# Kernel optimization log

Hardware: AMD Instinct MI355X
Metric: run time of the kernel (lower is better)

The kernel has to match this reference:

```python
import jax, jax.numpy as jnp
import numpy as np

B, T, D = 2, 2048, 1024
H, DH = 16, 64
E, K, F = 16, 2, 2048
CAP = 640  # ceil(B*T*K/E * 1.25)
DP, NPRIM = 256, 512
THETA = 10000.0
EPS = 1e-6


def rmsnorm(x, w):
    return x * jax.lax.rsqrt(jnp.mean(x * x, axis=-1, keepdims=True) + EPS) * w


def rope_attention(x, qkv_w, o_w):
    Bx, Tx, _ = x.shape
    qkv = (x @ qkv_w.T).reshape(Bx, Tx, 3, H, DH)
    q, k, v = qkv[:, :, 0], qkv[:, :, 1], qkv[:, :, 2]
    inv_freq = 1.0 / THETA ** (jnp.arange(0, DH, 2, dtype=jnp.float32) / DH)
    freqs = jnp.outer(jnp.arange(Tx, dtype=jnp.float32), inv_freq)
    emb = jnp.concatenate([freqs, freqs], axis=-1)
    cos = jnp.cos(emb)[None, :, None, :]  # [1,T,1,DH]
    sin = jnp.sin(emb)[None, :, None, :]

    def rot(u):
        u1, u2 = jnp.split(u, 2, axis=-1)
        return u * cos + jnp.concatenate([-u2, u1], axis=-1) * sin

    q, k = rot(q), rot(k)
    q, k, v = (z.transpose(0, 2, 1, 3) for z in (q, k, v))  # [B,H,T,DH]
    scores = jnp.einsum('bhqd,bhkd->bhqk', q, k) / np.sqrt(DH).astype(np.float32)
    causal = jnp.tril(jnp.ones((Tx, Tx), dtype=bool))
    scores = jnp.where(causal, scores, jnp.float32(-1e30))
    attn = jax.nn.softmax(scores, axis=-1)
    out = jnp.einsum('bhqk,bhkd->bhqd', attn, v).transpose(0, 2, 1, 3).reshape(Bx, Tx, D)
    return out @ o_w.T


def moe_layer(x, router_w, moe_w1, moe_w2):
    Bx, Tx, _ = x.shape
    N = Bx * Tx
    xf = x.reshape(N, D)
    logits = xf @ router_w.T                      # [N,E]
    probs = jax.nn.softmax(logits, axis=-1)
    topw, topi = jax.lax.top_k(probs, K)          # [N,K]
    topw = topw / jnp.sum(topw, axis=-1, keepdims=True)
    fi = topi.reshape(-1)                         # [N*K] expert ids
    fw = topw.reshape(-1)                         # [N*K] combine weights
    # sorted-dispatch emulation: position within each expert's buffer
    oh = jax.nn.one_hot(fi, E, dtype=jnp.int32)   # [N*K,E]
    pos = jnp.sum(jnp.cumsum(oh, axis=0) * oh, axis=-1) - 1
    keep = (pos < CAP).astype(xf.dtype)
    slot = jnp.minimum(pos, CAP - 1)
    xr = jnp.repeat(xf, K, axis=0)                # token-major, matches fi order
    buf = jnp.zeros((E, CAP, D), dtype=xf.dtype).at[fi, slot].add(xr * keep[:, None])
    # grouped GEMM per expert
    h = jax.nn.silu(jnp.einsum('ecd,edf->ecf', buf, moe_w1))
    yb = jnp.einsum('ecf,efd->ecd', h, moe_w2)
    # combine / scatter back
    yg = yb[fi, slot] * (keep * fw)[:, None]
    y = yg.reshape(N, K, D).sum(axis=1).reshape(Bx, Tx, D)
    # load-balancing aux loss
    frac = jnp.mean(oh.astype(jnp.float32).reshape(N, K, E).sum(axis=1), axis=0)
    pmean = jnp.mean(probs, axis=0)
    aux = jnp.float32(E) * jnp.sum(frac * pmean)
    return y, aux


def tou_cross_attn(x, prim, qw, kw, vw, ow, gw, gb):
    q = x @ qw.T                                   # [B,T,DP]
    k = prim @ kw.T                                # [N_PRIM,DP]
    v = prim @ vw.T
    attn = jax.nn.softmax(jnp.einsum('btp,np->btn', q, k) / np.sqrt(DP).astype(np.float32), axis=-1)
    out = jnp.einsum('btn,np->btp', attn, v) @ ow.T
    gate = jax.nn.sigmoid(x @ gw.T + gb)           # [B,T,1]
    return gate * out


def setup_inputs() -> dict:
    key = jax.random.key(0)
    ks = jax.random.split(key, 12)
    s = 0.02
    return {
        'x': jax.random.normal(ks[0], (B, T, D), dtype=jnp.float32),
        'tou_embeds': jax.random.normal(ks[1], (NPRIM, DP), dtype=jnp.float32),
        'norm1_w': jnp.ones((D,), jnp.float32),
        'qkv_w': jax.random.normal(ks[2], (3 * D, D), jnp.float32) * s,
        'attn_o_w': jax.random.normal(ks[3], (D, D), jnp.float32) * s,
        'norm2_w': jnp.ones((D,), jnp.float32),
        'router_w': jax.random.normal(ks[4], (E, D), jnp.float32) * s,
        'moe_w1': jax.random.normal(ks[5], (E, D, F), jnp.float32) * s,
        'moe_w2': jax.random.normal(ks[6], (E, F, D), jnp.float32) * s,
        'norm3_w': jnp.ones((D,), jnp.float32),
        'tou_q_w': jax.random.normal(ks[7], (DP, D), jnp.float32) * s,
        'tou_k_w': jax.random.normal(ks[8], (DP, DP), jnp.float32) * s,
        'tou_v_w': jax.random.normal(ks[9], (DP, DP), jnp.float32) * s,
        'tou_o_w': jax.random.normal(ks[10], (D, DP), jnp.float32) * s,
        'tou_gate_w': jax.random.normal(ks[11], (1, D), jnp.float32) * s,
        'tou_gate_b': jnp.zeros((1,), jnp.float32),
    }


def reference(x, tou_embeds, norm1_w, qkv_w, attn_o_w, norm2_w, router_w, moe_w1,
              moe_w2, norm3_w, tou_q_w, tou_k_w, tou_v_w, tou_o_w, tou_gate_w, tou_gate_b):
    x = x + rope_attention(rmsnorm(x, norm1_w), qkv_w, attn_o_w)
    moe_out, aux = moe_layer(rmsnorm(x, norm2_w), router_w, moe_w1, moe_w2)
    x = x + moe_out
    x = x + tou_cross_attn(rmsnorm(x, norm3_w), tou_embeds, tou_q_w, tou_k_w,
                           tou_v_w, tou_o_w, tou_gate_w, tou_gate_b)
    return (x, aux)
```

## Files before the change

kernel.cpp:

```cpp
#include <hip/hip_runtime.h>
#include <math.h>

typedef short bf16x8 __attribute__((ext_vector_type(8)));
typedef float f32x4 __attribute__((ext_vector_type(4)));

__device__ __forceinline__ unsigned short f2bf(float f) {
  union { float f; unsigned u; } v; v.f = f;
  return (unsigned short)((v.u + 0x7fff + ((v.u >> 16) & 1)) >> 16);
}
__device__ __forceinline__ float bf2f(unsigned short h) {
  union { unsigned u; float f; } v; v.u = ((unsigned)h) << 16;
  return v.f;
}

__device__ __forceinline__ void gld16(const unsigned short* g, unsigned short* l) {
  __builtin_amdgcn_global_load_lds((const __attribute__((address_space(1))) void*)g,
                                   (__attribute__((address_space(3))) void*)l, 16, 0, 0);
}

template <int WF32, int WLO>
__global__ __launch_bounds__(256) void rmsnorm_k(const float* __restrict__ x,
                                                 const float* __restrict__ w,
                                                 float* __restrict__ y,
                                                 unsigned short* __restrict__ yb,
                                                 unsigned short* __restrict__ yl) {
  const long n = blockIdx.x;
  const int t = threadIdx.x;
  const float4 v = ((const float4*)(x + n * 1024))[t];
  float ss = v.x * v.x + v.y * v.y + v.z * v.z + v.w * v.w;
#pragma unroll
  for (int o = 32; o > 0; o >>= 1) ss += __shfl_down(ss, o);
  __shared__ float red[4];
  __shared__ float sc;
  if ((t & 63) == 0) red[t >> 6] = ss;
  __syncthreads();
  if (t == 0) sc = rsqrtf((red[0] + red[1] + red[2] + red[3]) * (1.0f / 1024.0f) + 1e-6f);
  __syncthreads();
  const float s = sc;
  const float4 wv = ((const float4*)w)[t];
  float4 o;
  o.x = v.x * s * wv.x; o.y = v.y * s * wv.y; o.z = v.z * s * wv.z; o.w = v.w * s * wv.w;
  if (WF32) ((float4*)(y + n * 1024))[t] = o;
  ushort4 u = make_ushort4(f2bf(o.x), f2bf(o.y), f2bf(o.z), f2bf(o.w));
  *(ushort4*)(yb + n * 1024 + t * 4) = u;
  if (WLO) {
    ushort4 l = make_ushort4(f2bf(o.x - bf2f(u.x)), f2bf(o.y - bf2f(u.y)),
                             f2bf(o.z - bf2f(u.z)), f2bf(o.w - bf2f(u.w)));
    *(ushort4*)(yl + n * 1024 + t * 4) = l;
  }
}

__global__ __launch_bounds__(256) void split2_k(const float* __restrict__ s0,
                                                unsigned short* __restrict__ h0,
                                                unsigned short* __restrict__ l0,
                                                const float* __restrict__ s1,
                                                unsigned short* __restrict__ h1,
                                                unsigned short* __restrict__ l1) {
  const int i = blockIdx.x * 256 + threadIdx.x;
  const float* s; unsigned short* hp; unsigned short* lp; int off;
  if (i < 786432) { s = s0; hp = h0; lp = l0; off = i; }
  else            { s = s1; hp = h1; lp = l1; off = i - 786432; }
  const float4 v = ((const float4*)s)[off];
  ushort4 h = make_ushort4(f2bf(v.x), f2bf(v.y), f2bf(v.z), f2bf(v.w));
  ushort4 l = make_ushort4(f2bf(v.x - bf2f(h.x)), f2bf(v.y - bf2f(h.y)),
                           f2bf(v.z - bf2f(h.z)), f2bf(v.w - bf2f(h.w)));
  ((ushort4*)hp)[off] = h;
  ((ushort4*)lp)[off] = l;
}

__global__ __launch_bounds__(256) void cvt5_k(const float* __restrict__ s0, unsigned short* __restrict__ d0,
                                              const float* __restrict__ s1, unsigned short* __restrict__ d1,
                                              const float* __restrict__ s2, unsigned short* __restrict__ d2,
                                              const float* __restrict__ s3, unsigned short* __restrict__ d3,
                                              const float* __restrict__ s4, unsigned short* __restrict__ d4) {
  const int i = blockIdx.x * 256 + threadIdx.x;
  const float* s; unsigned short* d; int off;
  if (i < 65536)       { s = s0; d = d0; off = i; }
  else if (i < 81920)  { s = s1; d = d1; off = i - 65536; }
  else if (i < 98304)  { s = s2; d = d2; off = i - 81920; }
  else if (i < 163840) { s = s3; d = d3; off = i - 98304; }
  else                 { s = s4; d = d4; off = i - 163840; }
  const float4 v = ((const float4*)s)[off];
  ((ushort4*)d)[off] = make_ushort4(f2bf(v.x), f2bf(v.y), f2bf(v.z), f2bf(v.w));
}

__global__ __launch_bounds__(256) void cvt_t_k(const float* __restrict__ in,
                                               unsigned short* __restrict__ out,
                                               int R, int C) {
  in += (size_t)blockIdx.z * R * C;
  out += (size_t)blockIdx.z * R * C;
  const int r0 = blockIdx.y * 32, c0 = blockIdx.x * 32;
  __shared__ float T[32][33];
  const int tid = threadIdx.x;
  const int li = tid >> 3;
  const int lj = (tid & 7) << 2;
  const float4 v = *(const float4*)(in + (size_t)(r0 + li) * C + c0 + lj);
  T[li][lj + 0] = v.x; T[li][lj + 1] = v.y; T[li][lj + 2] = v.z; T[li][lj + 3] = v.w;
  __syncthreads();
  ushort4 u = make_ushort4(f2bf(T[lj + 0][li]), f2bf(T[lj + 1][li]),
                           f2bf(T[lj + 2][li]), f2bf(T[lj + 3][li]));
  *(ushort4*)(out + (size_t)(c0 + li) * R + r0 + lj) = u;
}

template <int MODE>
__global__ __launch_bounds__(256) void bgemm(const unsigned short* __restrict__ A,
                                             const unsigned short* __restrict__ B,
                                             void* __restrict__ Cv,
                                             int M, int N, int K,
                                             long sA, long sB, long sC, float alpha,
                                             const float* __restrict__ rowscale,
                                             const int* __restrict__ rowmap,
                                             const float* __restrict__ roww) {
  __shared__ __align__(16) unsigned short As[128 * 32];
  __shared__ __align__(16) unsigned short Bs[128 * 32];
  const int tid = threadIdx.x;
  const int z = blockIdx.z;
  const unsigned short* Ag = A + (size_t)z * sA;
  const unsigned short* Bg = B + (size_t)z * sB;
  const int m0 = blockIdx.y * 128, n0 = blockIdx.x * 128;
  const int lane = tid & 63;
  const int wid = tid >> 6;
  const int wm = (wid >> 1) * 64, wn = (wid & 1) * 64;
  const int fr = lane & 15, fq = lane >> 4;
  const int lr = tid >> 2, lk = (tid & 3) * 8;
  f32x4 acc[4][4] = {};
  const unsigned short* Ap0 = Ag + (size_t)(m0 + lr) * K + lk;
  const unsigned short* Ap1 = Ag + (size_t)(m0 + lr + 64) * K + lk;
  const unsigned short* Bp0 = Bg + (size_t)(n0 + lr) * K + lk;
  const unsigned short* Bp1 = Bg + (size_t)(n0 + lr + 64) * K + lk;
  unsigned short* Asw = As + wid * 512;
  unsigned short* Bsw = Bs + wid * 512;
  gld16(Ap0, Asw); gld16(Ap1, Asw + 2048);
  gld16(Bp0, Bsw); gld16(Bp1, Bsw + 2048);
  for (int k0 = 0;;) {
    __syncthreads();
    bf16x8 af[4], bv[4];
#pragma unroll
    for (int i = 0; i < 4; ++i) af[i] = *(const bf16x8*)&As[(wm + i * 16 + fr) * 32 + fq * 8];
#pragma unroll
    for (int j = 0; j < 4; ++j) bv[j] = *(const bf16x8*)&Bs[(wn + j * 16 + fr) * 32 + fq * 8];
    __syncthreads();
    k0 += 32;
    if (k0 < K) {
      gld16(Ap0 + k0, Asw); gld16(Ap1 + k0, Asw + 2048);
      gld16(Bp0 + k0, Bsw); gld16(Bp1 + k0, Bsw + 2048);
    }
#pragma unroll
    for (int i = 0; i < 4; ++i)
#pragma unroll
      for (int j = 0; j < 4; ++j)
        acc[i][j] = __builtin_amdgcn_mfma_f32_16x16x32_bf16(af[i], bv[j], acc[i][j], 0, 0, 0);
    if (k0 >= K) break;
  }
#pragma unroll
  for (int i = 0; i < 4; ++i) {
#pragma unroll
    for (int reg = 0; reg < 4; ++reg) {
      const int row = m0 + wm + i * 16 + fq * 4 + reg;
      float rs = 0.f, wgt = 0.f;
      int tok = -1;
      if (MODE == 4) rs = rowscale[row];
      if (MODE == 5) {
        tok = rowmap[z * M + row];
        if (tok >= 0) wgt = roww[z * M + row];
      }
#pragma unroll
      for (int j = 0; j < 4; ++j) {
        const int col = n0 + wn + j * 16 + fr;
        const float v = alpha * acc[i][j][reg];
        if (MODE == 0) {
          ((float*)Cv + (size_t)z * sC)[(size_t)row * N + col] = v;
        } else if (MODE == 1) {
          float* p = (float*)Cv + (size_t)z * sC + (size_t)row * N + col;
          *p += v;
        } else if (MODE == 2) {
          ((unsigned short*)Cv + (size_t)z * sC)[(size_t)row * N + col] = f2bf(v);
        } else if (MODE == 3) {
          const float sv = v / (1.f + expf(-v));
          ((unsigned short*)Cv + (size_t)z * sC)[(size_t)row * N + col] = f2bf(sv);
        } else if (MODE == 4) {
          float* p = (float*)Cv + (size_t)row * N + col;
          *p += rs * v;
        } else if (MODE == 5) {
          if (tok >= 0) atomicAdd((float*)Cv + (size_t)tok * N + col, wgt * v);
        }
      }
    }
  }
}

template <int MODE>
__global__ __launch_bounds__(256) void bgemm_s(const unsigned short* __restrict__ Ah,
                                               const unsigned short* __restrict__ Al,
                                               const unsigned short* __restrict__ Bh,
                                               const unsigned short* __restrict__ Bl,
                                               float* __restrict__ C,
                                               int M, int N, int K,
                                               const float* __restrict__ res,
                                               unsigned short* __restrict__ Qh,
                                               unsigned short* __restrict__ Ql,
                                               unsigned short* __restrict__ Kh,
                                               unsigned short* __restrict__ Kl,
                                               unsigned short* __restrict__ Vh,
                                               unsigned short* __restrict__ Vl) {
  __shared__ __align__(16) unsigned short Ash[128 * 32];
  __shared__ __align__(16) unsigned short Asl[128 * 32];
  __shared__ __align__(16) unsigned short Bsh[128 * 32];
  __shared__ __align__(16) unsigned short Bsl[128 * 32];
  const int tid = threadIdx.x;
  const int m0 = blockIdx.y * 128, n0 = blockIdx.x * 128;
  const int lane = tid & 63;
  const int wid = tid >> 6;
  const int wm = (wid >> 1) * 64, wn = (wid & 1) * 64;
  const int fr = lane & 15, fq = lane >> 4;
  const int lr = tid >> 2, lk = (tid & 3) * 8;
  f32x4 acc[4][4] = {};
  const size_t oA0 = (size_t)(m0 + lr) * K + lk, oA1 = (size_t)(m0 + lr + 64) * K + lk;
  const size_t oB0 = (size_t)(n0 + lr) * K + lk, oB1 = (size_t)(n0 + lr + 64) * K + lk;
  const int wb = wid * 512;
  gld16(Ah + oA0, Ash + wb); gld16(Ah + oA1, Ash + wb + 2048);
  gld16(Al + oA0, Asl + wb); gld16(Al + oA1, Asl + wb + 2048);
  gld16(Bh + oB0, Bsh + wb); gld16(Bh + oB1, Bsh + wb + 2048);
  gld16(Bl + oB0, Bsl + wb); gld16(Bl + oB1, Bsl + wb + 2048);
  for (int k0 = 0;;) {
    __syncthreads();
    bf16x8 afh[4], afl[4], bvh[4], bvl[4];
#pragma unroll
    for (int i = 0; i < 4; ++i) {
      afh[i] = *(const bf16x8*)&Ash[(wm + i * 16 + fr) * 32 + fq * 8];
      afl[i] = *(const bf16x8*)&Asl[(wm + i * 16 + fr) * 32 + fq * 8];
    }
#pragma unroll
    for (int j = 0; j < 4; ++j) {
      bvh[j] = *(const bf16x8*)&Bsh[(wn + j * 16 + fr) * 32 + fq * 8];
      bvl[j] = *(const bf16x8*)&Bsl[(wn + j * 16 + fr) * 32 + fq * 8];
    }
    __syncthreads();
    k0 += 32;
    if (k0 < K) {
      gld16(Ah + oA0 + k0, Ash + wb); gld16(Ah + oA1 + k0, Ash + wb + 2048);
      gld16(Al + oA0 + k0, Asl + wb); gld16(Al + oA1 + k0, Asl + wb + 2048);
      gld16(Bh + oB0 + k0, Bsh + wb); gld16(Bh + oB1 + k0, Bsh + wb + 2048);
      gld16(Bl + oB0 + k0, Bsl + wb); gld16(Bl + oB1 + k0, Bsl + wb + 2048);
    }
#pragma unroll
    for (int j = 0; j < 4; ++j) {
#pragma unroll
      for (int i = 0; i < 4; ++i) {
        acc[i][j] = __builtin_amdgcn_mfma_f32_16x16x32_bf16(afl[i], bvh[j], acc[i][j], 0, 0, 0);
        acc[i][j] = __builtin_amdgcn_mfma_f32_16x16x32_bf16(afh[i], bvl[j], acc[i][j], 0, 0, 0);
        acc[i][j] = __builtin_amdgcn_mfma_f32_16x16x32_bf16(afh[i], bvh[j], acc[i][j], 0, 0, 0);
      }
    }
    if (k0 >= K) break;
  }
  if (MODE == 3) {
    const int band = n0 + wn;
    const int which = band >> 10;
    const int h = (band & 1023) >> 6;
    unsigned short* Hp = (which == 0) ? Qh : ((which == 1) ? Kh : Vh);
    unsigned short* Lp = (which == 0) ? Ql : ((which == 1) ? Kl : Vl);
    const float l2t = 13.287712379549449f;
    const float inv0 = exp2f(-l2t * (float)fr * (1.0f / 32.0f));
    const float inv1 = exp2f(-l2t * (float)(fr + 16) * (1.0f / 32.0f));
#pragma unroll
    for (int i = 0; i < 4; ++i) {
#pragma unroll
      for (int reg = 0; reg < 4; ++reg) {
        const int row = m0 + wm + i * 16 + fq * 4 + reg;
        const int b = row >> 11, t = row & 2047;
        float o0 = acc[i][0][reg], o1 = acc[i][1][reg];
        float o2 = acc[i][2][reg], o3 = acc[i][3][reg];
        if (which != 2) {
          const float a0 = (float)t * inv0, a1 = (float)t * inv1;
          const float c0 = cosf(a0), sn0 = sinf(a0);
          const float c1 = cosf(a1), sn1 = sinf(a1);
          const float v0 = o0, v1 = o1, v2 = o2, v3 = o3;
          o0 = v0 * c0 - v2 * sn0;
          o1 = v1 * c1 - v3 * sn1;
          o2 = v2 * c0 + v0 * sn0;
          o3 = v3 * c1 + v1 * sn1;
        }
        const long bo = ((long)((b << 4) + h) * 2048 + t) * 64 + fr;
        const unsigned short h0 = f2bf(o0), h1 = f2bf(o1);
        const unsigned short h2 = f2bf(o2), h3 = f2bf(o3);
        Hp[bo] = h0; Hp[bo + 16] = h1; Hp[bo + 32] = h2; Hp[bo + 48] = h3;
        Lp[bo]      = f2bf(o0 - bf2f(h0));
        Lp[bo + 16] = f2bf(o1 - bf2f(h1));
        Lp[bo + 32] = f2bf(o2 - bf2f(h2));
        Lp[bo + 48] = f2bf(o3 - bf2f(h3));
      }
    }
  } else {
#pragma unroll
    for (int i = 0; i < 4; ++i) {
#pragma unroll
      for (int reg = 0; reg < 4; ++reg) {
        const int row = m0 + wm + i * 16 + fq * 4 + reg;
#pragma unroll
        for (int j = 0; j < 4; ++j) {
          const int col = n0 + wn + j * 16 + fr;
          float* p = C + (size_t)row * N + col;
          if (MODE == 0) *p = acc[i][j][reg];
          else if (MODE == 1) *p += acc[i][j][reg];
          else *p = res[(size_t)row * N + col] + acc[i][j][reg];
        }
      }
    }
  }
}

__global__ __launch_bounds__(256) void flash_k(const unsigned short* __restrict__ Qhg,
                                               const unsigned short* __restrict__ Qlg,
                                               const unsigned short* __restrict__ Khg,
                                               const unsigned short* __restrict__ Klg,
                                               const unsigned short* __restrict__ Vhg,
                                               const unsigned short* __restrict__ Vlg,
                                               unsigned short* __restrict__ axh,
                                               unsigned short* __restrict__ axl) {
  const int qb = (int)gridDim.x - 1 - (int)blockIdx.x;
  const int bh = blockIdx.y;
  const int b = bh >> 4, h = bh & 15;
  const int q0 = qb << 6;
  __shared__ __align__(16) unsigned short Ksh[64 * 64];
  __shared__ __align__(16) unsigned short Ksl[64 * 64];
  __shared__ __align__(16) unsigned short Vth[64 * 64];
  __shared__ __align__(16) unsigned short Vtl[64 * 64];
  __shared__ __align__(16) unsigned short Psh[4 * 16 * 64];
  __shared__ __align__(16) unsigned short Psl[4 * 16 * 64];
  const int tid = threadIdx.x;
  const int w = tid >> 6;
  const int lane = tid & 63;
  const int fr = lane & 15, fq = lane >> 4;
  const long base_q = ((long)bh * 2048 + q0) * 64;
  bf16x8 qh_r[2], ql_r[2];
#pragma unroll
  for (int kc = 0; kc < 2; ++kc) {
    qh_r[kc] = *(const bf16x8*)(Qhg + base_q + (w * 16 + fr) * 64 + kc * 32 + fq * 8);
    ql_r[kc] = *(const bf16x8*)(Qlg + base_q + (w * 16 + fr) * 64 + kc * 32 + fq * 8);
  }
  f32x4 o_acc[4] = {};
  float m_st[4], l_st[4];
#pragma unroll
  for (int i = 0; i < 4; ++i) { m_st[i] = -3.0e38f; l_st[i] = 0.f; }

  uint4 vhr[2], vlr[2];

  {
    const long bk = (long)bh * 2048 * 64;
#pragma unroll
    for (int rep = 0; rep < 2; ++rep) {
      const int f = tid + rep * 256;
      const int r = f >> 3, c = f & 7;
      const long src = bk + r * 64 + ((c ^ (r & 7)) * 8);
      gld16(Khg + src, Ksh + f * 8);
      gld16(Klg + src, Ksl + f * 8);
    }
#pragma unroll
    for (int rep = 0; rep < 2; ++rep) {
      const int f = tid + rep * 256;
      const int t = f >> 3, d0 = (f & 7) * 8;
      vhr[rep] = *(const uint4*)(Vhg + bk + t * 64 + d0);
      vlr[rep] = *(const uint4*)(Vlg + bk + t * 64 + d0);
    }
#pragma unroll
    for (int rep = 0; rep < 2; ++rep) {
      const int f = tid + rep * 256;
      const int t = f >> 3, d0 = (f & 7) * 8;
      unsigned uh[4] = {vhr[rep].x, vhr[rep].y, vhr[rep].z, vhr[rep].w};
      unsigned ul[4] = {vlr[rep].x, vlr[rep].y, vlr[rep].z, vlr[rep].w};
#pragma unroll
      for (int i2 = 0; i2 < 4; ++i2) {
        const int de = d0 + 2 * i2, doo = de + 1;
        Vth[de * 64 + (t ^ ((2 * i2) << 3))] = (unsigned short)(uh[i2] & 0xffff);
        Vth[doo * 64 + (t ^ ((2 * i2 + 1) << 3))] = (unsigned short)(uh[i2] >> 16);
        Vtl[de * 64 + (t ^ ((2 * i2) << 3))] = (unsigned short)(ul[i2] & 0xffff);
        Vtl[doo * 64 + (t ^ ((2 * i2 + 1) << 3))] = (unsigned short)(ul[i2] >> 16);
      }
    }
    __syncthreads();
  }

  for (int kb = 0;; ++kb) {
    const bool more = (kb < qb);
    const long bk_next = ((long)bh * 2048 + ((kb + 1) << 6)) * 64;
    f32x4 sfr[4] = {};
    __builtin_amdgcn_s_setprio(1);
#pragma unroll
    for (int kc = 0; kc < 2; ++kc) {
#pragma unroll
      for (int j = 0; j < 4; ++j) {
        const int co = (j * 16 + fr) * 64 + ((kc * 32 + fq * 8) ^ ((fr & 7) << 3));
        const bf16x8 kh_ = *(const bf16x8*)&Ksh[co];
        const bf16x8 kl_ = *(const bf16x8*)&Ksl[co];
        sfr[j] = __builtin_amdgcn_mfma_f32_16x16x32_bf16(ql_r[kc], kh_, sfr[j], 0, 0, 0);
        sfr[j] = __builtin_amdgcn_mfma_f32_16x16x32_bf16(qh_r[kc], kl_, sfr[j], 0, 0, 0);
        sfr[j] = __builtin_amdgcn_mfma_f32_16x16x32_bf16(qh_r[kc], kh_, sfr[j], 0, 0, 0);
      }
    }
    __builtin_amdgcn_s_setprio(0);
    if (more) {
#pragma unroll
      for (int rep = 0; rep < 2; ++rep) {
        const int f = tid + rep * 256;
        const int t = f >> 3, d0 = (f & 7) * 8;
        vhr[rep] = *(const uint4*)(Vhg + bk_next + t * 64 + d0);
        vlr[rep] = *(const uint4*)(Vlg + bk_next + t * 64 + d0);
      }
    }
    const bool diag = (kb == qb);
    float p[4][4];
    float alpha[4];
#pragma unroll
    for (int reg = 0; reg < 4; ++reg) {
      const int qloc = w * 16 + fq * 4 + reg;
      float v[4];
#pragma unroll
      for (int j = 0; j < 4; ++j) {
        float s = sfr[j][reg] * 0.125f;
        if (diag && (j * 16 + fr) > qloc) s = -1.0e30f;
        v[j] = s;
      }
      float mt = fmaxf(fmaxf(v[0], v[1]), fmaxf(v[2], v[3]));
#pragma unroll
      for (int off = 1; off < 16; off <<= 1) mt = fmaxf(mt, __shfl_xor(mt, off));
      const float mn = fmaxf(m_st[reg], mt);
      alpha[reg] = expf(m_st[reg] - mn);
      m_st[reg] = mn;
      float ps = 0.f;
#pragma unroll
      for (int j = 0; j < 4; ++j) { p[j][reg] = expf(v[j] - mn); ps += p[j][reg]; }
#pragma unroll
      for (int off = 1; off < 16; off <<= 1) ps += __shfl_xor(ps, off);
      l_st[reg] = l_st[reg] * alpha[reg] + ps;
    }
#pragma unroll
    for (int reg = 0; reg < 4; ++reg) {
      const int qp = fq * 4 + reg;
#pragma unroll
      for (int j = 0; j < 4; ++j) {
        const float pv = p[j][reg];
        const unsigned short ph = f2bf(pv);
        const unsigned short pl = f2bf(pv - bf2f(ph));
        const int sa = w * 1024 + qp * 64 + ((j * 16 + fr) ^ ((qp & 7) << 3));
        Psh[sa] = ph;
        Psl[sa] = pl;
      }
    }
#pragma unroll
    for (int j = 0; j < 4; ++j)
#pragma unroll
      for (int reg = 0; reg < 4; ++reg) o_acc[j][reg] *= alpha[reg];
    __syncthreads();
    if (more) {
#pragma unroll
      for (int rep = 0; rep < 2; ++rep) {
        const int f = tid + rep * 256;
        const int r = f >> 3, c = f & 7;
        const long src = bk_next + r * 64 + ((c ^ (r & 7)) * 8);
        gld16(Khg + src, Ksh + f * 8);
        gld16(Klg + src, Ksl + f * 8);
      }
    }
    __builtin_amdgcn_s_setprio(1);
#pragma unroll
    for (int kc = 0; kc < 2; ++kc) {
      const int po = w * 1024 + fr * 64 + ((kc * 32 + fq * 8) ^ ((fr & 7) << 3));
      const bf16x8 ph_ = *(const bf16x8*)&Psh[po];
      const bf16x8 pl_ = *(const bf16x8*)&Psl[po];
#pragma unroll
      for (int j = 0; j < 4; ++j) {
        const int co = (j * 16 + fr) * 64 + ((kc * 32 + fq * 8) ^ ((fr & 7) << 3));
        const bf16x8 vh_ = *(const bf16x8*)&Vth[co];
        const bf16x8 vl_ = *(const bf16x8*)&Vtl[co];
        o_acc[j] = __builtin_amdgcn_mfma_f32_16x16x32_bf16(pl_, vh_, o_acc[j], 0, 0, 0);
        o_acc[j] = __builtin_amdgcn_mfma_f32_16x16x32_bf16(ph_, vl_, o_acc[j], 0, 0, 0);
        o_acc[j] = __builtin_amdgcn_mfma_f32_16x16x32_bf16(ph_, vh_, o_acc[j], 0, 0, 0);
      }
    }
    __builtin_amdgcn_s_setprio(0);
    if (!more) break;
    __syncthreads();
#pragma unroll
    for (int rep = 0; rep < 2; ++rep) {
      const int f = tid + rep * 256;
      const int t = f >> 3, d0 = (f & 7) * 8;
      unsigned uh[4] = {vhr[rep].x, vhr[rep].y, vhr[rep].z, vhr[rep].w};
      unsigned ul[4] = {vlr[rep].x, vlr[rep].y, vlr[rep].z, vlr[rep].w};
#pragma unroll
      for (int i2 = 0; i2 < 4; ++i2) {
        const int de = d0 + 2 * i2, doo = de + 1;
        Vth[de * 64 + (t ^ ((2 * i2) << 3))] = (unsigned short)(uh[i2] & 0xffff);
        Vth[doo * 64 + (t ^ ((2 * i2 + 1) << 3))] = (unsigned short)(uh[i2] >> 16);
        Vtl[de * 64 + (t ^ ((2 * i2) << 3))] = (unsigned short)(ul[i2] & 0xffff);
        Vtl[doo * 64 + (t ^ ((2 * i2 + 1) << 3))] = (unsigned short)(ul[i2] >> 16);
      }
    }
  }
#pragma unroll
  for (int reg = 0; reg < 4; ++reg) {
    const long tok = (long)b * 2048 + q0 + w * 16 + fq * 4 + reg;
    const float il = 1.f / l_st[reg];
#pragma unroll
    for (int j = 0; j < 4; ++j) {
      const float v = o_acc[j][reg] * il;
      const unsigned short hi = f2bf(v);
      const unsigned short lo = f2bf(v - bf2f(hi));
      const long off = tok * 1024 + h * 64 + j * 16 + fr;
      axh[off] = hi;
      axl[off] = lo;
    }
  }
}

__global__ __launch_bounds__(256) void router_k(const float* __restrict__ xn,
                                                const float* __restrict__ rw,
                                                int* __restrict__ topi,
                                                float* __restrict__ topw,
                                                float* __restrict__ probs) {
  const int n = blockIdx.x;
  const int t = threadIdx.x;
  const float4 xv = ((const float4*)(xn + (size_t)n * 1024))[t];
  float acc[16];
#pragma unroll
  for (int e = 0; e < 16; ++e) {
    const float4 wv = ((const float4*)(rw + (size_t)e * 1024))[t];
    acc[e] = xv.x * wv.x + xv.y * wv.y + xv.z * wv.z + xv.w * wv.w;
  }
#pragma unroll
  for (int e = 0; e < 16; ++e)
#pragma unroll
    for (int o = 32; o > 0; o >>= 1) acc[e] += __shfl_down(acc[e], o);
  __shared__ float red[4][16];
  if ((t & 63) == 0) {
#pragma unroll
    for (int e = 0; e < 16; ++e) red[t >> 6][e] = acc[e];
  }
  __syncthreads();
  if (t == 0) {
    float logits[16];
#pragma unroll
    for (int e = 0; e < 16; ++e)
      logits[e] = red[0][e] + red[1][e] + red[2][e] + red[3][e];
    float mx = logits[0];
#pragma unroll
    for (int e = 1; e < 16; ++e) mx = fmaxf(mx, logits[e]);
    float p[16];
    float Z = 0.f;
#pragma unroll
    for (int e = 0; e < 16; ++e) { p[e] = expf(logits[e] - mx); Z += p[e]; }
    const float iz = 1.f / Z;
#pragma unroll
    for (int e = 0; e < 16; ++e) p[e] *= iz;
    int i1 = 0;
#pragma unroll
    for (int e = 1; e < 16; ++e) if (p[e] > p[i1]) i1 = e;
    int i2 = (i1 == 0) ? 1 : 0;
#pragma unroll
    for (int e = 0; e < 16; ++e) if (e != i1 && p[e] > p[i2]) i2 = e;
    const float sw = p[i1] + p[i2];
    topi[2 * n] = i1; topi[2 * n + 1] = i2;
    topw[2 * n] = p[i1] / sw; topw[2 * n + 1] = p[i2] / sw;
    float* pr = probs + (size_t)n * 16;
#pragma unroll
    for (int e = 0; e < 16; ++e) pr[e] = p[e];
  }
}

__global__ __launch_bounds__(256) void psum_k(const float* __restrict__ probs,
                                              float* __restrict__ psum) {
  float acc[16] = {};
  for (int n = threadIdx.x; n < 4096; n += 256) {
    const float4* pr = (const float4*)(probs + (size_t)n * 16);
#pragma unroll
    for (int q = 0; q < 4; ++q) {
      const float4 v = pr[q];
      acc[q * 4 + 0] += v.x; acc[q * 4 + 1] += v.y;
      acc[q * 4 + 2] += v.z; acc[q * 4 + 3] += v.w;
    }
  }
#pragma unroll
  for (int e = 0; e < 16; ++e)
#pragma unroll
    for (int o = 32; o > 0; o >>= 1) acc[e] += __shfl_down(acc[e], o);
  __shared__ float red[4][16];
  if ((threadIdx.x & 63) == 0) {
#pragma unroll
    for (int e = 0; e < 16; ++e) red[threadIdx.x >> 6][e] = acc[e];
  }
  __syncthreads();
  if (threadIdx.x < 16)
    psum[threadIdx.x] = red[0][threadIdx.x] + red[1][threadIdx.x] +
                        red[2][threadIdx.x] + red[3][threadIdx.x];
}

__global__ __launch_bounds__(256) void pos_k(const int* __restrict__ topi,
                                             const float* __restrict__ topw,
                                             int* __restrict__ slot,
                                             int* __restrict__ keep,
                                             int* __restrict__ s2t,
                                             float* __restrict__ s2w,
                                             float* __restrict__ cnt) {
  __shared__ int fi[8192];
  __shared__ int hist[256][16];
  __shared__ int total[16];
  const int t = threadIdx.x;
  for (int i = t; i < 8192; i += 256) fi[i] = topi[i];
#pragma unroll
  for (int e = 0; e < 16; ++e) hist[t][e] = 0;
  __syncthreads();
  const int base = t * 32;
#pragma unroll 8
  for (int i = 0; i < 32; ++i) hist[t][fi[base + i]]++;
  __syncthreads();
  if (t < 16) {
    int run = 0;
    for (int c = 0; c < 256; ++c) { const int v = hist[c][t]; hist[c][t] = run; run += v; }
    total[t] = run;
    cnt[t] = (float)run;
  }
  __syncthreads();
  int run[16];
#pragma unroll
  for (int e = 0; e < 16; ++e) run[e] = hist[t][e];
  for (int i = 0; i < 32; ++i) {
    const int idx = base + i;
    const int e = fi[idx];
    const int p = run[e]++;
    if (p < 640) {
      slot[idx] = p; keep[idx] = 1;
      s2t[e * 640 + p] = idx >> 1;
      s2w[e * 640 + p] = topw[idx];
    } else {
      slot[idx] = 639; keep[idx] = 0;
    }
  }
  __syncthreads();
  for (int pos = t; pos < 16 * 640; pos += 256) {
    const int e = pos / 640, c = pos - e * 640;
    if (c >= total[e]) s2t[pos] = -1;
  }
}

__global__ __launch_bounds__(128) void scatter_b_k(const unsigned short* __restrict__ xnb,
                                                   const int* __restrict__ topi,
                                                   const int* __restrict__ slot,
                                                   const int* __restrict__ keep,
                                                   unsigned short* __restrict__ buf) {
  const int i = blockIdx.x;
  if (!keep[i]) return;
  const int n = i >> 1;
  const size_t dst = ((size_t)topi[i] * 640 + slot[i]) * 1024;
  ((uint4*)(buf + dst))[threadIdx.x] = ((const uint4*)(xnb + (size_t)n * 1024))[threadIdx.x];
}

__global__ void aux_k(const float* __restrict__ cnt, const float* __restrict__ psum,
                      float* __restrict__ out) {
  if (threadIdx.x == 0) {
    float s = 0.f;
    for (int e = 0; e < 16; ++e)
      s += (cnt[e] * (1.f / 4096.f)) * (psum[e] * (1.f / 4096.f));
    out[0] = 16.f * s;
  }
}

__global__ __launch_bounds__(256) void softmax512_k(const float* __restrict__ sc,
                                                    unsigned short* __restrict__ out) {
  const long n = blockIdx.x;
  const float2* row = (const float2*)(sc + n * 512);
  const int t = threadIdx.x;
  float2 v = row[t];
  float mx = fmaxf(v.x, v.y);
#pragma unroll
  for (int o = 32; o > 0; o >>= 1) mx = fmaxf(mx, __shfl_down(mx, o));
  __shared__ float red[4];
  __shared__ float bm, bz;
  if ((t & 63) == 0) red[t >> 6] = mx;
  __syncthreads();
  if (t == 0) bm = fmaxf(fmaxf(red[0], red[1]), fmaxf(red[2], red[3]));
  __syncthreads();
  const float M = bm;
  const float e0 = expf(v.x - M), e1 = expf(v.y - M);
  float s = e0 + e1;
#pragma unroll
  for (int o = 32; o > 0; o >>= 1) s += __shfl_down(s, o);
  if ((t & 63) == 0) red[t >> 6] = s;
  __syncthreads();
  if (t == 0) bz = 1.f / (red[0] + red[1] + red[2] + red[3]);
  __syncthreads();
  ushort2 u; u.x = f2bf(e0 * bz); u.y = f2bf(e1 * bz);
  *(ushort2*)(out + n * 512 + t * 2) = u;
}

__global__ __launch_bounds__(256) void gate_k(const float* __restrict__ xn,
                                              const float* __restrict__ gw,
                                              const float* __restrict__ gb,
                                              float* __restrict__ gate) {
  const long n = blockIdx.x;
  const int t = threadIdx.x;
  const float4 v = ((const float4*)(xn + n * 1024))[t];
  const float4 g = ((const float4*)gw)[t];
  float s = v.x * g.x + v.y * g.y + v.z * g.z + v.w * g.w;
#pragma unroll
  for (int o = 32; o > 0; o >>= 1) s += __shfl_down(s, o);
  __shared__ float red[4];
  if ((t & 63) == 0) red[t >> 6] = s;
  __syncthreads();
  if (t == 0) {
    const float tot = red[0] + red[1] + red[2] + red[3] + gb[0];
    gate[n] = 1.f / (1.f + expf(-tot));
  }
}

extern "C" void kernel_launch(void* const* d_in, const int* in_sizes, int n_in,
                              void* d_out, int out_size, void* d_ws, size_t ws_size,
                              hipStream_t stream) {
  (void)in_sizes; (void)n_in; (void)out_size; (void)ws_size;
  const float* x    = (const float*)d_in[0];
  const float* prim = (const float*)d_in[1];
  const float* n1w  = (const float*)d_in[2];
  const float* qkvw = (const float*)d_in[3];
  const float* aow  = (const float*)d_in[4];
  const float* n2w  = (const float*)d_in[5];
  const float* rw   = (const float*)d_in[6];
  const float* w1   = (const float*)d_in[7];
  const float* w2   = (const float*)d_in[8];
  const float* n3w  = (const float*)d_in[9];
  const float* tqw  = (const float*)d_in[10];
  const float* tkw  = (const float*)d_in[11];
  const float* tvw  = (const float*)d_in[12];
  const float* tow  = (const float*)d_in[13];
  const float* tgw  = (const float*)d_in[14];
  const float* tgb  = (const float*)d_in[15];

  float* xbuf = (float*)d_out;
  float* aux  = xbuf + 4194304;

  char* W = (char*)d_ws;
  float* xn            = (float*)W;
  unsigned short* xnb  = (unsigned short*)(W + (16u << 20));
  unsigned short* xnl  = (unsigned short*)(W + (24u << 20));
  char* P = W + (32u << 20);

  unsigned short* qh   = (unsigned short*)(P + (48u << 20));
  unsigned short* ql   = (unsigned short*)(P + (56u << 20));
  unsigned short* kh   = (unsigned short*)(P + (64u << 20));
  unsigned short* kl   = (unsigned short*)(P + (72u << 20));
  unsigned short* vh   = (unsigned short*)(P + (80u << 20));
  unsigned short* vl   = (unsigned short*)(P + (88u << 20));
  unsigned short* axh  = (unsigned short*)(P + (112u << 20));
  unsigned short* axl  = (unsigned short*)(P + (120u << 20));
  unsigned short* qwh  = (unsigned short*)(P + (128u << 20));
  unsigned short* qwl  = (unsigned short*)(P + (134u << 20));
  unsigned short* aoh  = (unsigned short*)(P + (140u << 20));
  unsigned short* aol  = (unsigned short*)(P + (142u << 20));
  int*   topi = (int*)P;
  float* topw = (float*)(P + 65536);
  int*   slot = (int*)(P + 131072);
  int*   keep = (int*)(P + 196608);
  float* cnt  = (float*)(P + 262144);
  float* psum = (float*)(P + 262144 + 4096);
  int*   s2t  = (int*)(P + 327680);
  float* s2w  = (float*)(P + 393216);
  float* probs = (float*)(P + 458752);
  unsigned short* bufb = (unsigned short*)(P + (1u << 20));
  unsigned short* hb   = (unsigned short*)(P + (22u << 20));
  unsigned short* Wt   = (unsigned short*)(P + (64u << 20));
  unsigned short* tqb  = (unsigned short*)P;
  unsigned short* tkb  = (unsigned short*)(P + (2u << 20));
  unsigned short* tvtb = (unsigned short*)(P + (3u << 20));
  float*          tsc  = (float*)(P + (4u << 20));
  unsigned short* tpb  = (unsigned short*)(P + (12u << 20));
  unsigned short* tavb = (unsigned short*)(P + (16u << 20));
  float*          gate = (float*)(P + (18u << 20));
  unsigned short* tqwb = (unsigned short*)(P + (19u << 20));
  unsigned short* tkwb = (unsigned short*)(P + (20u << 20));
  unsigned short* tvwb = (unsigned short*)(P + (21u << 20));
  unsigned short* towb = (unsigned short*)(P + (22u << 20));
  unsigned short* primb= (unsigned short*)(P + (23u << 20));

  rmsnorm_k<0, 1><<<4096, 256, 0, stream>>>(x, n1w, nullptr, xnb, xnl);
  split2_k<<<4096, 256, 0, stream>>>(qkvw, qwh, qwl, aow, aoh, aol);
  bgemm_s<3><<<dim3(24, 32, 1), 256, 0, stream>>>(xnb, xnl, qwh, qwl, nullptr,
      4096, 3072, 1024, nullptr, qh, ql, kh, kl, vh, vl);
  flash_k<<<dim3(32, 32), 256, 0, stream>>>(qh, ql, kh, kl, vh, vl, axh, axl);
  bgemm_s<2><<<dim3(8, 32, 1), 256, 0, stream>>>(axh, axl, aoh, aol, xbuf,
      4096, 1024, 1024, x, nullptr, nullptr, nullptr, nullptr, nullptr, nullptr);

  rmsnorm_k<1, 0><<<4096, 256, 0, stream>>>(xbuf, n2w, xn, xnb, nullptr);
  router_k<<<4096, 256, 0, stream>>>(xn, rw, topi, topw, probs);
  psum_k<<<1, 256, 0, stream>>>(probs, psum);
  pos_k<<<1, 256, 0, stream>>>(topi, topw, slot, keep, s2t, s2w, cnt);
  scatter_b_k<<<8192, 128, 0, stream>>>(xnb, topi, slot, keep, bufb);
  cvt_t_k<<<dim3(64, 32, 16), 256, 0, stream>>>(w1, Wt, 1024, 2048);
  bgemm<3><<<dim3(16, 5, 16), 256, 0, stream>>>(bufb, Wt, hb, 640, 2048, 1024,
      (long)640 * 1024, (long)2048 * 1024, (long)640 * 2048, 1.f, nullptr, nullptr, nullptr);
  cvt_t_k<<<dim3(32, 64, 16), 256, 0, stream>>>(w2, Wt, 2048, 1024);
  bgemm<5><<<dim3(8, 5, 16), 256, 0, stream>>>(hb, Wt, xbuf, 640, 1024, 2048,
      (long)640 * 2048, (long)1024 * 2048, 0, 1.f, nullptr, s2t, s2w);
  aux_k<<<1, 64, 0, stream>>>(cnt, psum, aux);

  rmsnorm_k<1, 0><<<4096, 256, 0, stream>>>(xbuf, n3w, xn, xnb, nullptr);
  cvt5_k<<<768, 256, 0, stream>>>(tqw, tqwb, tkw, tkwb, tvw, tvwb, tow, towb, prim, primb);
  bgemm<2><<<dim3(2, 32, 1), 256, 0, stream>>>(xnb, tqwb, tqb, 4096, 256, 1024, 0, 0, 0, 1.f, nullptr, nullptr, nullptr);
  bgemm<2><<<dim3(2, 4, 1), 256, 0, stream>>>(primb, tkwb, tkb, 512, 256, 256, 0, 0, 0, 1.f, nullptr, nullptr, nullptr);
  bgemm<2><<<dim3(4, 2, 1), 256, 0, stream>>>(tvwb, primb, tvtb, 256, 512, 256, 0, 0, 0, 1.f, nullptr, nullptr, nullptr);
  bgemm<0><<<dim3(4, 32, 1), 256, 0, stream>>>(tqb, tkb, tsc, 4096, 512, 256, 0, 0, 0, 0.0625f, nullptr, nullptr, nullptr);
  softmax512_k<<<4096, 256, 0, stream>>>(tsc, tpb);
  bgemm<2><<<dim3(2, 32, 1), 256, 0, stream>>>(tpb, tvtb, tavb, 4096, 256, 512, 0, 0, 0, 1.f, nullptr, nullptr, nullptr);
  gate_k<<<4096, 256, 0, stream>>>(xn, tgw, tgb, gate);
  bgemm<4><<<dim3(8, 32, 1), 256, 0, stream>>>(tavb, towb, xbuf, 4096, 1024, 256, 0, 0, 0, 1.f, gate, nullptr, nullptr);
}
```

Measured before the change: 1.089 ms.

## Pre-transpose V in a separate kernel and async-load it into flash attention

Adds a kernel that transposes the bf16 hi/lo V tensors to [bh, d, t] layout before attention. The flash kernel then loads V tiles straight into LDS with global_load_lds, like K, instead of loading them into registers and scattering transposed shorts into LDS each iteration. This removes the register staging and the scattered LDS writes, at the cost of an extra launch and an extra pass over V through memory. It also swaps expf for the faster, less precise __expf in the softmax and the SiLU epilogue.

New measurement: 962.5 us. -11.6%, faster.

```diff
diff --git a/kernel.cpp b/kernel.cpp
--- a/kernel.cpp
+++ b/kernel.cpp
@@ -100,6 +100,25 @@
   ushort4 u = make_ushort4(f2bf(T[lj + 0][li]), f2bf(T[lj + 1][li]),
                            f2bf(T[lj + 2][li]), f2bf(T[lj + 3][li]));
   *(ushort4*)(out + (size_t)(c0 + li) * R + r0 + lj) = u;
+}
+
+__global__ __launch_bounds__(256) void cvt_tb_k(const unsigned short* __restrict__ in0,
+                                                unsigned short* __restrict__ out0,
+                                                const unsigned short* __restrict__ in1,
+                                                unsigned short* __restrict__ out1) {
+  const int zz = blockIdx.z;
+  const unsigned short* in = (zz < 32 ? in0 : in1) + (size_t)(zz & 31) * 2048 * 64;
+  unsigned short* out = (zz < 32 ? out0 : out1) + (size_t)(zz & 31) * 2048 * 64;
+  const int r0 = blockIdx.y * 32, c0 = blockIdx.x * 32;
+  __shared__ unsigned short T[32][36];
+  const int tid = threadIdx.x;
+  const int li = tid >> 3;
+  const int lj = (tid & 7) << 2;
+  const ushort4 v = *(const ushort4*)(in + (size_t)(r0 + li) * 64 + c0 + lj);
+  T[li][lj + 0] = v.x; T[li][lj + 1] = v.y; T[li][lj + 2] = v.z; T[li][lj + 3] = v.w;
+  __syncthreads();
+  ushort4 u = make_ushort4(T[lj + 0][li], T[lj + 1][li], T[lj + 2][li], T[lj + 3][li]);
+  *(ushort4*)(out + (size_t)(c0 + li) * 2048 + r0 + lj) = u;
 }
 
 template <int MODE>
@@ -176,7 +195,7 @@
         } else if (MODE == 2) {
           ((unsigned short*)Cv + (size_t)z * sC)[(size_t)row * N + col] = f2bf(v);
         } else if (MODE == 3) {
-          const float sv = v / (1.f + expf(-v));
+          const float sv = v / (1.f + __expf(-v));
           ((unsigned short*)Cv + (size_t)z * sC)[(size_t)row * N + col] = f2bf(sv);
         } else if (MODE == 4) {
           float* p = (float*)Cv + (size_t)row * N + col;
@@ -314,8 +333,8 @@
                                                const unsigned short* __restrict__ Qlg,
                                                const unsigned short* __restrict__ Khg,
                                                const unsigned short* __restrict__ Klg,
-                                               const unsigned short* __restrict__ Vhg,
-                                               const unsigned short* __restrict__ Vlg,
+                                               const unsigned short* __restrict__ Vthg,
+                                               const unsigned short* __restrict__ Vtlg,
                                                unsigned short* __restrict__ axh,
                                                unsigned short* __restrict__ axl) {
   const int qb = (int)gridDim.x - 1 - (int)blockIdx.x;
@@ -333,6 +352,7 @@
   const int lane = tid & 63;
   const int fr = lane & 15, fq = lane >> 4;
   const long base_q = ((long)bh * 2048 + q0) * 64;
+  const long kv_base = (long)bh * 2048 * 64;
   bf16x8 qh_r[2], ql_r[2];
 #pragma unroll
   for (int kc = 0; kc < 2; ++kc) {
@@ -344,46 +364,23 @@
 #pragma unroll
   for (int i = 0; i < 4; ++i) { m_st[i] = -3.0e38f; l_st[i] = 0.f; }
 
-  uint4 vhr[2], vlr[2];
-
   {
-    const long bk = (long)bh * 2048 * 64;
 #pragma unroll
     for (int rep = 0; rep < 2; ++rep) {
       const int f = tid + rep * 256;
       const int r = f >> 3, c = f & 7;
-      const long src = bk + r * 64 + ((c ^ (r & 7)) * 8);
-      gld16(Khg + src, Ksh + f * 8);
-      gld16(Klg + src, Ksl + f * 8);
-    }
-#pragma unroll
-    for (int rep = 0; rep < 2; ++rep) {
-      const int f = tid + rep * 256;
-      const int t = f >> 3, d0 = (f & 7) * 8;
-      vhr[rep] = *(const uint4*)(Vhg + bk + t * 64 + d0);
-      vlr[rep] = *(const uint4*)(Vlg + bk + t * 64 + d0);
-    }
-#pragma unroll
-    for (int rep = 0; rep < 2; ++rep) {
-      const int f = tid + rep * 256;
-      const int t = f >> 3, d0 = (f & 7) * 8;
-      unsigned uh[4] = {vhr[rep].x, vhr[rep].y, vhr[rep].z, vhr[rep].w};
-      unsigned ul[4] = {vlr[rep].x, vlr[rep].y, vlr[rep].z, vlr[rep].w};
-#pragma unroll
-      for (int i2 = 0; i2 < 4; ++i2) {
-        const int de = d0 + 2 * i2, doo = de + 1;
-        Vth[de * 64 + (t ^ ((2 * i2) << 3))] = (unsigned short)(uh[i2] & 0xffff);
-        Vth[doo * 64 + (t ^ ((2 * i2 + 1) << 3))] = (unsigned short)(uh[i2] >> 16);
-        Vtl[de * 64 + (t ^ ((2 * i2) << 3))] = (unsigned short)(ul[i2] & 0xffff);
-        Vtl[doo * 64 + (t ^ ((2 * i2 + 1) << 3))] = (unsigned short)(ul[i2] >> 16);
-      }
+      const long srcK = kv_base + r * 64 + ((c ^ (r & 7)) * 8);
+      gld16(Khg + srcK, Ksh + f * 8);
+      gld16(Klg + srcK, Ksl + f * 8);
+      const long srcV = kv_base + (long)r * 2048 + ((c ^ (r & 7)) * 8);
+      gld16(Vthg + srcV, Vth + f * 8);
+      gld16(Vtlg + srcV, Vtl + f * 8);
     }
     __syncthreads();
   }
 
   for (int kb = 0;; ++kb) {
     const bool more = (kb < qb);
-    const long bk_next = ((long)bh * 2048 + ((kb + 1) << 6)) * 64;
     f32x4 sfr[4] = {};
     __builtin_amdgcn_s_setprio(1);
 #pragma unroll
@@ -399,15 +396,6 @@
       }
     }
     __builtin_amdgcn_s_setprio(0);
-    if (more) {
-#pragma unroll
-      for (int rep = 0; rep < 2; ++rep) {
-        const int f = tid + rep * 256;
-        const int t = f >> 3, d0 = (f & 7) * 8;
-        vhr[rep] = *(const uint4*)(Vhg + bk_next + t * 64 + d0);
-        vlr[rep] = *(const uint4*)(Vlg + bk_next + t * 64 + d0);
-      }
-    }
     const bool diag = (kb == qb);
     float p[4][4];
     float alpha[4];
@@ -425,11 +413,11 @@
 #pragma unroll
       for (int off = 1; off < 16; off <<= 1) mt = fmaxf(mt, __shfl_xor(mt, off));
       const float mn = fmaxf(m_st[reg], mt);
-      alpha[reg] = expf(m_st[reg] - mn);
+      alpha[reg] = __expf(m_st[reg] - mn);
       m_st[reg] = mn;
       float ps = 0.f;
 #pragma unroll
-      for (int j = 0; j < 4; ++j) { p[j][reg] = expf(v[j] - mn); ps += p[j][reg]; }
+      for (int j = 0; j < 4; ++j) { p[j][reg] = __expf(v[j] - mn); ps += p[j][reg]; }
 #pragma unroll
       for (int off = 1; off < 16; off <<= 1) ps += __shfl_xor(ps, off);
       l_st[reg] = l_st[reg] * alpha[reg] + ps;
@@ -453,11 +441,12 @@
       for (int reg = 0; reg < 4; ++reg) o_acc[j][reg] *= alpha[reg];
     __syncthreads();
     if (more) {
+      const long bk = kv_base + (long)((kb + 1) << 6) * 64;
 #pragma unroll
       for (int rep = 0; rep < 2; ++rep) {
         const int f = tid + rep * 256;
         const int r = f >> 3, c = f & 7;
-        const long src = bk_next + r * 64 + ((c ^ (r & 7)) * 8);
+        const long src = bk + r * 64 + ((c ^ (r & 7)) * 8);
         gld16(Khg + src, Ksh + f * 8);
         gld16(Klg + src, Ksl + f * 8);
       }
@@ -481,19 +470,15 @@
     __builtin_amdgcn_s_setprio(0);
     if (!more) break;
     __syncthreads();
-#pragma unroll
-    for (int rep = 0; rep < 2; ++rep) {
-      const int f = tid + rep * 256;
-      const int t = f >> 3, d0 = (f & 7) * 8;
-      unsigned uh[4] = {vhr[rep].x, vhr[rep].y, vhr[rep].z, vhr[rep].w};
-      unsigned ul[4] = {vlr[rep].x, vlr[rep].y, vlr[rep].z, vlr[rep].w};
-#pragma unroll
-      for (int i2 = 0; i2 < 4; ++i2) {
-        const int de = d0 + 2 * i2, doo = de + 1;
-        Vth[de * 64 + (t ^ ((2 * i2) << 3))] = (unsigned short)(uh[i2] & 0xffff);
-        Vth[doo * 64 + (t ^ ((2 * i2 + 1) << 3))] = (unsigned short)(uh[i2] >> 16);
-        Vtl[de * 64 + (t ^ ((2 * i2) << 3))] = (unsigned short)(ul[i2] & 0xffff);
-        Vtl[doo * 64 + (t ^ ((2 * i2 + 1) << 3))] = (unsigned short)(ul[i2] >> 16);
+    {
+      const int t0 = (kb + 1) << 6;
+#pragma unroll
+      for (int rep = 0; rep < 2; ++rep) {
+        const int f = tid + rep * 256;
+        const int d = f >> 3, c = f & 7;
+        const long src = kv_base + (long)d * 2048 + t0 + ((c ^ (d & 7)) * 8);
+        gld16(Vthg + src, Vth + f * 8);
+        gld16(Vtlg + src, Vtl + f * 8);
       }
     }
   }
@@ -748,6 +733,8 @@
   unsigned short* kl   = (unsigned short*)(P + (72u << 20));
   unsigned short* vh   = (unsigned short*)(P + (80u << 20));
   unsigned short* vl   = (unsigned short*)(P + (88u << 20));
+  unsigned short* vth  = (unsigned short*)(P + (96u << 20));
+  unsigned short* vtl  = (unsigned short*)(P + (104u << 20));
   unsigned short* axh  = (unsigned short*)(P + (112u << 20));
   unsigned short* axl  = (unsigned short*)(P + (120u << 20));
   unsigned short* qwh  = (unsigned short*)(P + (128u << 20));
@@ -783,7 +770,8 @@
   split2_k<<<4096, 256, 0, stream>>>(qkvw, qwh, qwl, aow, aoh, aol);
   bgemm_s<3><<<dim3(24, 32, 1), 256, 0, stream>>>(xnb, xnl, qwh, qwl, nullptr,
       4096, 3072, 1024, nullptr, qh, ql, kh, kl, vh, vl);
-  flash_k<<<dim3(32, 32), 256, 0, stream>>>(qh, ql, kh, kl, vh, vl, axh, axl);
+  cvt_tb_k<<<dim3(2, 64, 64), 256, 0, stream>>>(vh, vth, vl, vtl);
+  flash_k<<<dim3(32, 32), 256, 0, stream>>>(qh, ql, kh, kl, vth, vtl, axh, axl);
   bgemm_s<2><<<dim3(8, 32, 1), 256, 0, stream>>>(axh, axl, aoh, aol, xbuf,
       4096, 1024, 1024, x, nullptr, nullptr, nullptr, nullptr, nullptr, nullptr);
 
```
